# Kernel optimization log

Hardware: AMD Instinct MI355X
Metric: run time of the kernel (lower is better)

Reference implementation:

```python
import jax, jax.numpy as jnp
from jax import lax
import numpy as np

NUM_COEFF = 24      # solver.num_coeff_per_dim (Chebyshev coefficients)
NUM_POINTS = 48     # Chebyshev-Gauss collocation nodes per interval
PICARD_ITERS = 5    # fixed-point iterations of the spectral PAN solve


def _cheb_setup(dtype):
    j = jnp.arange(NUM_POINTS, dtype=dtype)
    n = jnp.arange(NUM_COEFF, dtype=dtype)
    # tau_j = cos(pi*(j+1/2)/P); T[n, j] = T_n(tau_j) = cos(n*arccos(tau_j))
    ang = jnp.pi * (j + 0.5) / NUM_POINTS
    T = jnp.cos(n[:, None] * ang[None, :])                  # [C, P]
    V = (2.0 / NUM_POINTS) * T
    V = V.at[0].mul(0.5)                                    # DCT: a_n = sum_j f(tau_j) V[n, j]
    signs = jnp.cos(n * jnp.pi)                             # T_n(-1) = (-1)^n
    return T, V, signs


def _cheb_antiderivative(a, signs):
    # Chebyshev coeffs of int_{-1}^{tau} f, given coeffs a of f: b_n = (a_{n-1}-a_{n+1})/(2n)
    C = a.shape[-1]
    a_pad = jnp.concatenate([a, jnp.zeros_like(a[..., :2])], axis=-1)
    n = jnp.arange(1, C, dtype=a.dtype)
    b_rest = (a_pad[..., 0:C - 1] - a_pad[..., 2:C + 1]) / (2.0 * n)
    b0 = -jnp.sum(b_rest * signs[1:], axis=-1, keepdims=True)  # enforce value 0 at tau=-1
    return jnp.concatenate([b0, b_rest], axis=-1)


def _vf(y, W1, b1, W2, b2):
    # neural vector field f(t, y): autonomous MLP
    return jnp.tanh(y @ W1 + b1) @ W2 + b2


def _pan_solve(y_init, t_span, W1, b1, W2, b2):
    # Chebyshev-spectral (PAN) ODE solve; returns trajectory at t_span points
    # and the per-interval coefficient tensors B_all [I, batch, dim, C]
    T, V, signs = _cheb_setup(y_init.dtype)

    def solve_interval(y0, ts):
        t0, t1 = ts[0], ts[1]
        scale = (t1 - t0) * 0.5                             # dtau -> dt Jacobian

        def picard(B, _):
            y_nodes = jnp.einsum('bdc,cp->pbd', B, T)       # y at collocation nodes
            fvals = _vf(y_nodes, W1, b1, W2, b2)            # [P, batch, dim]
            a = jnp.einsum('pbd,cp->bdc', fvals, V)         # Chebyshev coeffs of f
            Bn = scale * _cheb_antiderivative(a, signs)
            Bn = Bn.at[..., 0].add(y0)                      # y(tau=-1) = y0
            return Bn, None

        B0 = jnp.zeros((*y0.shape, NUM_COEFF), y0.dtype).at[..., 0].set(y0)
        B, _ = lax.scan(picard, B0, None, length=PICARD_ITERS)
        y1 = jnp.sum(B, axis=-1)                            # T_n(1) = 1
        return y1, (B, y1)

    ts = jnp.stack([t_span[:-1], t_span[1:]], axis=-1)      # [I, 2]
    _, (B_all, y_ends) = lax.scan(solve_interval, y_init, ts)
    traj = jnp.concatenate([y_init[None], y_ends], axis=0)  # [I+1, batch, dim]
    return traj, B_all


def setup_inputs() -> dict:
    key = jax.random.key(0)
    k1, k2, k3 = jax.random.split(key, 3)
    batch, dim, hidden = 256, 512, 512
    s = np.float32(1.0 / np.sqrt(dim))
    return {
        'y_init': jax.random.normal(k1, (batch, dim), jnp.float32),
        't_span': jnp.linspace(0.0, 1.0, 7, dtype=jnp.float32),
        'W1': s * jax.random.normal(k2, (dim, hidden), jnp.float32),
        'b1': jnp.zeros((hidden,), jnp.float32),
        'W2': s * jax.random.normal(k3, (hidden, dim), jnp.float32),
        'b2': jnp.zeros((dim,), jnp.float32),
    }


def reference(y_init, t_span, W1, b1, W2, b2):
    traj, _B_all = _pan_solve(y_init, t_span, W1, b1, W2, b2)
    return (t_span, traj)
```

## Files before the change

kernel.cpp:

```cpp
#include <hip/hip_runtime.h>
#include <hip/hip_bf16.h>
#include <math.h>

#define NC 24
#define NP 48
#define NI 6
#define BATCH 256
#define DIM 512
#define NROW (NP*BATCH)
#define NELEM (BATCH*DIM)

typedef __bf16 bf16x8 __attribute__((ext_vector_type(8)));
typedef float f32x4 __attribute__((ext_vector_type(4)));
using bf16 = __hip_bfloat16;

struct bq8 { __hip_bfloat162 a, b; };

__device__ __forceinline__ void gld_lds16(const void* g, void* l) {
  __builtin_amdgcn_global_load_lds(
      (const __attribute__((address_space(1))) void*)g,
      (__attribute__((address_space(3))) void*)l, 16, 0, 0);
}

__device__ __forceinline__ float fast_tanh(float x) {
  float u = __expf(2.0f * x);
  float r = __builtin_amdgcn_rcpf(u + 1.0f);
  return __builtin_fmaf(-2.0f, r, 1.0f);
}

__global__ void k_setup(const float* __restrict__ t_span, bf16* __restrict__ Mbf,
                        float* __restrict__ wv, float* __restrict__ rs,
                        float* __restrict__ scales, float* __restrict__ zbias,
                        float* __restrict__ out) {
  __shared__ double Tsh[NC][NP];
  __shared__ float Msh[NP][NP];
  __shared__ float wsh[NP];
  int tid = threadIdx.x;
  for (int idx = tid; idx < NC*NP; idx += 64) {
    int c = idx / NP, p = idx % NP;
    Tsh[c][p] = cos((double)c * (M_PI * ((double)p + 0.5) / NP));
  }
  for (int idx = tid; idx < NP*64; idx += 64)
    Mbf[idx] = __float2bfloat16(0.f);
  __syncthreads();
  if (tid < NP) {
    int q = tid;
    double V[NC], K[NC];
    for (int c = 0; c < NC; c++) V[c] = (2.0/NP) * Tsh[c][q];
    V[0] *= 0.5;
    double s = 0.0;
    for (int n = 1; n < NC; n++) {
      double hi = (n+1 < NC) ? V[n+1] : 0.0;
      K[n] = (V[n-1] - hi) / (2.0*n);
      s += (n & 1) ? -K[n] : K[n];
    }
    K[0] = -s;
    double wsum = 0.0;
    for (int c = 0; c < NC; c++) wsum += K[c];
    wv[q] = (float)wsum;
    wsh[q] = (float)wsum;
    for (int p = 0; p < NP; p++) {
      double m = 0.0;
      for (int c = 0; c < NC; c++) m += Tsh[c][p] * K[c];
      Msh[p][q] = (float)m;
      Mbf[p*64 + q] = __float2bfloat16((float)m);
    }
  }
  __syncthreads();
  if (tid < NP) {
    float s = 0.f;
    for (int q = 0; q < NP; q++) s += Msh[tid][q];
    rs[tid] = s;
  }
  if (tid == 0) {
    float s = 0.f;
    for (int q = 0; q < NP; q++) s += wsh[q];
    scales[6] = s;
  }
  for (int idx = tid; idx < DIM; idx += 64) zbias[idx] = 0.f;
  if (tid < NI) scales[tid] = 0.5f*(t_span[tid+1]-t_span[tid]);
  if (tid < NI+1) out[tid] = t_span[tid];
}

__global__ void k_wt(const float* __restrict__ W1, const float* __restrict__ W2,
                     bf16* __restrict__ W1T, bf16* __restrict__ W2T,
                     bf16* __restrict__ W2bf) {
  int idx = blockIdx.x*256 + threadIdx.x;
  int k = idx >> 9, n = idx & 511;
  W1T[n*DIM + k] = __float2bfloat16(W1[idx]);
  W2T[n*DIM + k] = __float2bfloat16(W2[idx]);
  W2bf[idx]      = __float2bfloat16(W2[idx]);
}

__global__ void k_bb(const float* __restrict__ W1, const float* __restrict__ b2,
                     float* __restrict__ bb) {
  int h = blockIdx.x*256 + threadIdx.x;
  float s = 0.f;
  for (int d = 0; d < DIM; d++) s = fmaf(b2[d], W1[d*DIM + h], s);
  bb[h] = s;
}

__global__ void k_init(const float* __restrict__ y_init, float* __restrict__ y0,
                       bf16* __restrict__ y0bf, float* __restrict__ traj0) {
  int i = blockIdx.x*256 + threadIdx.x;
  float v = y_init[i];
  y0[i] = v; traj0[i] = v;
  y0bf[i] = __float2bfloat16(v);
}

template<int EPI>
__global__ __launch_bounds__(256, 3) void k_gemm(const bf16* __restrict__ A,
    const bf16* __restrict__ BT, const float* __restrict__ bias,
    bf16* __restrict__ outb, float* __restrict__ outf) {
  __shared__ bf16 sA[2][128*64];
  __shared__ bf16 sB[2][64*64];
  int tid = threadIdx.x;
  int lane = tid & 63, wid = tid >> 6;
  int q8 = gridDim.x >> 3;
  int tl = (blockIdx.x & 7)*q8 + (blockIdx.x >> 3);
  int bm = tl >> 3, bn = tl & 7;
  int row0 = bm*128, col0 = bn*64;
  int wr = wid >> 1, wc = wid & 1;
  int r16 = lane & 15, g = lane >> 4;

  f32x4 acc[4][2];
  #pragma unroll
  for (int m = 0; m < 4; m++)
    #pragma unroll
    for (int n = 0; n < 2; n++)
      acc[m][n] = {0.f, 0.f, 0.f, 0.f};

  auto stage = [&](int buf, int k0) {
    #pragma unroll
    for (int j = 0; j < 4; j++) {
      int cid = wid*64 + lane + j*256;
      int r = cid >> 3;
      int c = (cid & 7) ^ (r & 7);
      gld_lds16(A + (size_t)(row0 + r)*DIM + k0 + c*8,
                (char*)&sA[buf][0] + wid*1024 + j*4096);
    }
    #pragma unroll
    for (int j = 0; j < 2; j++) {
      int cid = wid*64 + lane + j*256;
      int r = cid >> 3;
      int c = (cid & 7) ^ (r & 7);
      gld_lds16(BT + (size_t)(col0 + r)*DIM + k0 + c*8,
                (char*)&sB[buf][0] + wid*1024 + j*4096);
    }
  };

  stage(0, 0);
  int cur = 0;
  for (int k0 = 0; k0 < DIM; k0 += 64) {
    if (k0 + 64 < DIM) {
      stage(cur ^ 1, k0 + 64);
      asm volatile("s_waitcnt vmcnt(6)" ::: "memory");
    } else {
      asm volatile("s_waitcnt vmcnt(0)" ::: "memory");
    }
    __builtin_amdgcn_s_barrier();
    #pragma unroll
    for (int kk = 0; kk < 2; kk++) {
      bf16x8 af[4], bfr[2];
      #pragma unroll
      for (int m = 0; m < 4; m++) {
        int r = wr*64 + m*16 + r16;
        af[m] = *(const bf16x8*)(&sA[cur][0] + r*64 + (((kk*4+g) ^ (r&7))*8));
      }
      #pragma unroll
      for (int n = 0; n < 2; n++) {
        int r = wc*32 + n*16 + r16;
        bfr[n] = *(const bf16x8*)(&sB[cur][0] + r*64 + (((kk*4+g) ^ (r&7))*8));
      }
      #pragma unroll
      for (int m = 0; m < 4; m++)
        #pragma unroll
        for (int n = 0; n < 2; n++)
          acc[m][n] = __builtin_amdgcn_mfma_f32_16x16x32_bf16(af[m], bfr[n], acc[m][n], 0, 0, 0);
    }
    __builtin_amdgcn_s_barrier();
    cur ^= 1;
  }

  #pragma unroll
  for (int m = 0; m < 4; m++) {
    int rowb = row0 + wr*64 + m*16 + g*4;
    #pragma unroll
    for (int n = 0; n < 2; n++) {
      int col = col0 + wc*32 + n*16 + r16;
      float bv = bias[col];
      #pragma unroll
      for (int r = 0; r < 4; r++) {
        float v = acc[m][n][r] + bv;
        size_t idx = (size_t)(rowb + r)*DIM + col;
        if constexpr (EPI == 1) {
          outb[idx] = __float2bfloat16(v);
        } else {
          outf[idx] = v;
          outb[idx] = __float2bfloat16(fast_tanh(v));
        }
      }
    }
  }
}

template<int FIN>
__global__ __launch_bounds__(256, 2) void k_fused(const bf16* __restrict__ H,
    const bf16* __restrict__ W21T, const float* __restrict__ C,
    const bf16* __restrict__ Mbf, const float* __restrict__ rs,
    const float* __restrict__ bb, const float* __restrict__ wv,
    const float* __restrict__ scales, int t, bf16* __restrict__ outp) {
  __shared__ char smem[57344];
  bf16* sA = (bf16*)smem;
  bf16* sB = (bf16*)(smem + 24576);
  char* sGT = smem;
  int tid = threadIdx.x;
  int lane = tid & 63, wid = tid >> 6;
  int q8 = gridDim.x >> 3;
  int tl = (blockIdx.x & 7)*q8 + (blockIdx.x >> 3);
  int bm = tl >> 2, bn = tl & 3;
  int row0 = bm*96, col0 = bn*128;
  int b_w = wid >> 1;
  int wr0 = b_w*48, wc0 = (wid & 1)*64;
  int r16 = lane & 15, g = lane >> 4;

  bf16x8 af2[3][2];
  #pragma unroll
  for (int pt = 0; pt < 3; pt++)
    #pragma unroll
    for (int kk = 0; kk < 2; kk++)
      af2[pt][kk] = *(const bf16x8*)(Mbf + (pt*16 + r16)*64 + kk*32 + g*8);

  f32x4 acc[3][4];
  #pragma unroll
  for (int m = 0; m < 3; m++)
    #pragma unroll
    for (int n = 0; n < 4; n++)
      acc[m][n] = {0.f, 0.f, 0.f, 0.f};

  auto stage = [&](int buf, int k0) {
    #pragma unroll
    for (int j = 0; j < 3; j++) {
      int cid = j*256 + tid;
      int r = cid >> 3;
      int c = (cid & 7) ^ (r & 7);
      gld_lds16(H + (size_t)(row0 + r)*DIM + k0 + c*8,
                (char*)(sA + buf*6144) + j*4096 + wid*1024);
    }
    #pragma unroll
    for (int j = 0; j < 4; j++) {
      int cid = j*256 + tid;
      int r = cid >> 3;
      int c = (cid & 7) ^ (r & 7);
      gld_lds16(W21T + (size_t)(col0 + r)*DIM + k0 + c*8,
                (char*)(sB + buf*8192) + j*4096 + wid*1024);
    }
  };

  stage(0, 0);
  int cur = 0;
  for (int k0 = 0; k0 < DIM; k0 += 64) {
    if (k0 + 64 < DIM) {
      stage(cur ^ 1, k0 + 64);
      asm volatile("s_waitcnt vmcnt(7)" ::: "memory");
    } else {
      asm volatile("s_waitcnt vmcnt(0)" ::: "memory");
    }
    __builtin_amdgcn_s_barrier();
    #pragma unroll
    for (int kk = 0; kk < 2; kk++) {
      bf16x8 af[3], bfr[4];
      #pragma unroll
      for (int m = 0; m < 3; m++) {
        int r = wr0 + m*16 + r16;
        af[m] = *(const bf16x8*)(sA + cur*6144 + r*64 + (((kk*4+g) ^ (r&7))*8));
      }
      #pragma unroll
      for (int n = 0; n < 4; n++) {
        int r = wc0 + n*16 + r16;
        bfr[n] = *(const bf16x8*)(sB + cur*8192 + r*64 + (((kk*4+g) ^ (r&7))*8));
      }
      #pragma unroll
      for (int m = 0; m < 3; m++)
        #pragma unroll
        for (int n = 0; n < 4; n++)
          acc[m][n] = __builtin_amdgcn_mfma_f32_16x16x32_bf16(af[m], bfr[n], acc[m][n], 0, 0, 0);
    }
    __builtin_amdgcn_s_barrier();
    cur ^= 1;
  }

  __syncthreads();
  #pragma unroll
  for (int m = 0; m < 3; m++) {
    int qb = m*16 + g*4;
    #pragma unroll
    for (int n = 0; n < 4; n++) {
      int h_loc = wc0 + n*16 + r16;
      int ad = (h_loc*256 + b_w*128 + qb*2) ^ ((h_loc&7)<<4);
      bq8 v;
      v.a = __hip_bfloat162{__float2bfloat16(acc[m][n][0]), __float2bfloat16(acc[m][n][1])};
      v.b = __hip_bfloat162{__float2bfloat16(acc[m][n][2]), __float2bfloat16(acc[m][n][3])};
      *(bq8*)(sGT + ad) = v;
    }
  }
  {
    int hz = tid >> 1, bz = tid & 1;
    bq8 z; z.a = __hip_bfloat162{__float2bfloat16(0.f), __float2bfloat16(0.f)}; z.b = z.a;
    #pragma unroll
    for (int j = 0; j < 4; j++) {
      int ad = (hz*256 + bz*128 + 96 + j*8) ^ ((hz&7)<<4);
      *(bq8*)(sGT + ad) = z;
    }
  }
  __syncthreads();

  int hh = wid & 1;
  f32x4 acc2[3][4];
  #pragma unroll
  for (int m = 0; m < 3; m++)
    #pragma unroll
    for (int n = 0; n < 4; n++)
      acc2[m][n] = {0.f, 0.f, 0.f, 0.f};
  #pragma unroll
  for (int kk = 0; kk < 2; kk++) {
    bf16x8 bfr2[4];
    #pragma unroll
    for (int n2 = 0; n2 < 4; n2++) {
      int h_loc = hh*64 + n2*16 + r16;
      int ad = (h_loc*256 + b_w*128 + (kk*32 + g*8)*2) ^ ((h_loc&7)<<4);
      bfr2[n2] = *(const bf16x8*)(sGT + ad);
    }
    #pragma unroll
    for (int pt = 0; pt < 3; pt++)
      #pragma unroll
      for (int n2 = 0; n2 < 4; n2++)
        acc2[pt][n2] = __builtin_amdgcn_mfma_f32_16x16x32_bf16(af2[pt][kk], bfr2[n2], acc2[pt][n2], 0, 0, 0);
  }

  float sc = scales[t];
  int bglob = bm*2 + b_w;
  float rsv[3][4];
  #pragma unroll
  for (int pt = 0; pt < 3; pt++)
    #pragma unroll
    for (int r = 0; r < 4; r++)
      rsv[pt][r] = rs[pt*16 + g*4 + r];

  #pragma unroll
  for (int n2 = 0; n2 < 4; n2++) {
    int h_glob = col0 + hh*64 + n2*16 + r16;
    float cv = C[(size_t)bglob*DIM + h_glob];
    float bbv = bb[h_glob];
    if constexpr (FIN == 0) {
      #pragma unroll
      for (int pt = 0; pt < 3; pt++) {
        #pragma unroll
        for (int r = 0; r < 4; r++) {
          int p = pt*16 + g*4 + r;
          float z = fmaf(sc, fmaf(rsv[pt][r], bbv, acc2[pt][n2][r]), cv);
          outp[((size_t)bglob*NP + p)*DIM + h_glob] = __float2bfloat16(fast_tanh(z));
        }
      }
    } else {
      float hw = 0.f;
      #pragma unroll
      for (int pt = 0; pt < 3; pt++) {
        #pragma unroll
        for (int r = 0; r < 4; r++) {
          int p = pt*16 + g*4 + r;
          float z = fmaf(sc, fmaf(rsv[pt][r], bbv, acc2[pt][n2][r]), cv);
          hw = fmaf(wv[p], fast_tanh(z), hw);
        }
      }
      hw += __shfl_xor(hw, 16);
      hw += __shfl_xor(hw, 32);
      if (g == 0)
        outp[(size_t)bglob*DIM + h_glob] = __float2bfloat16(hw);
    }
  }
}

__global__ __launch_bounds__(256, 3) void k_next(const bf16* __restrict__ A,
    const bf16* __restrict__ W2T, const bf16* __restrict__ W21T,
    const float* __restrict__ b2, const float* __restrict__ bb,
    float* __restrict__ y0, bf16* __restrict__ y0bf, float* __restrict__ C,
    bf16* __restrict__ H1, const float* __restrict__ scales, int t,
    float* __restrict__ traj) {
  __shared__ bf16 sA[2][128*64];
  __shared__ bf16 sB[2][64*64];
  int tid = threadIdx.x;
  int lane = tid & 63, wid = tid >> 6;
  int q8 = gridDim.x >> 3;
  int tl = (blockIdx.x & 7)*q8 + (blockIdx.x >> 3);
  int bm = tl >> 4, bn = tl & 15;
  int half = bn >> 3;
  int row0 = bm*128, col0 = (bn & 7)*64;
  const bf16* BT = half ? W21T : W2T;
  int wr = wid >> 1, wc = wid & 1;
  int r16 = lane & 15, g = lane >> 4;

  f32x4 acc[4][2];
  #pragma unroll
  for (int m = 0; m < 4; m++)
    #pragma unroll
    for (int n = 0; n < 2; n++)
      acc[m][n] = {0.f, 0.f, 0.f, 0.f};

  auto stage = [&](int buf, int k0) {
    #pragma unroll
    for (int j = 0; j < 4; j++) {
      int cid = wid*64 + lane + j*256;
      int r = cid >> 3;
      int c = (cid & 7) ^ (r & 7);
      gld_lds16(A + (size_t)(row0 + r)*DIM + k0 + c*8,
                (char*)&sA[buf][0] + wid*1024 + j*4096);
    }
    #pragma unroll
    for (int j = 0; j < 2; j++) {
      int cid = wid*64 + lane + j*256;
      int r = cid >> 3;
      int c = (cid & 7) ^ (r & 7);
      gld_lds16(BT + (size_t)(col0 + r)*DIM + k0 + c*8,
                (char*)&sB[buf][0] + wid*1024 + j*4096);
    }
  };

  stage(0, 0);
  int cur = 0;
  for (int k0 = 0; k0 < DIM; k0 += 64) {
    if (k0 + 64 < DIM) {
      stage(cur ^ 1, k0 + 64);
      asm volatile("s_waitcnt vmcnt(6)" ::: "memory");
    } else {
      asm volatile("s_waitcnt vmcnt(0)" ::: "memory");
    }
    __builtin_amdgcn_s_barrier();
    #pragma unroll
    for (int kk = 0; kk < 2; kk++) {
      bf16x8 af[4], bfr[2];
      #pragma unroll
      for (int m = 0; m < 4; m++) {
        int r = wr*64 + m*16 + r16;
        af[m] = *(const bf16x8*)(&sA[cur][0] + r*64 + (((kk*4+g) ^ (r&7))*8));
      }
      #pragma unroll
      for (int n = 0; n < 2; n++) {
        int r = wc*32 + n*16 + r16;
        bfr[n] = *(const bf16x8*)(&sB[cur][0] + r*64 + (((kk*4+g) ^ (r&7))*8));
      }
      #pragma unroll
      for (int m = 0; m < 4; m++)
        #pragma unroll
        for (int n = 0; n < 2; n++)
          acc[m][n] = __builtin_amdgcn_mfma_f32_16x16x32_bf16(af[m], bfr[n], acc[m][n], 0, 0, 0);
    }
    __builtin_amdgcn_s_barrier();
    cur ^= 1;
  }

  float sc = scales[t];
  float sumw = scales[6];
  #pragma unroll
  for (int m = 0; m < 4; m++) {
    int rowb = row0 + wr*64 + m*16 + g*4;
    #pragma unroll
    for (int n = 0; n < 2; n++) {
      int col = col0 + wc*32 + n*16 + r16;
      #pragma unroll
      for (int r = 0; r < 4; r++) {
        size_t idx = (size_t)(rowb + r)*DIM + col;
        if (half == 0) {
          float bv = sumw * b2[col];
          float y1 = fmaf(sc, acc[m][n][r] + bv, y0[idx]);
          y0[idx] = y1;
          y0bf[idx] = __float2bfloat16(y1);
          traj[idx] = y1;
        } else {
          float cb = sc * sumw * bb[col];
          float cnew = fmaf(sc, acc[m][n][r], C[idx] + cb);
          C[idx] = cnew;
          H1[idx] = __float2bfloat16(fast_tanh(cnew));
        }
      }
    }
  }
}

__global__ __launch_bounds__(256) void k_combine1(const bf16* __restrict__ G1,
    const float* __restrict__ C, const float* __restrict__ rs,
    const float* __restrict__ bb, const float* __restrict__ scales, int t,
    bf16* __restrict__ outH) {
  int i = (blockIdx.x*256 + threadIdx.x)*2;
  int b = i >> 9, h = i & (DIM-1);
  __hip_bfloat162 gb = *(const __hip_bfloat162*)(G1 + i);
  float2 c = *(const float2*)(C + i);
  float g0 = __bfloat162float(gb.x) + bb[h];
  float g1 = __bfloat162float(gb.y) + bb[h+1];
  float sc = scales[t];
  #pragma unroll
  for (int p = 0; p < NP; p++) {
    float w = sc * rs[p];
    __hip_bfloat162 o;
    o.x = __float2bfloat16(fast_tanh(fmaf(w, g0, c.x)));
    o.y = __float2bfloat16(fast_tanh(fmaf(w, g1, c.y)));
    *(__hip_bfloat162*)(outH + ((size_t)b*NP + p)*DIM + h) = o;
  }
}

extern "C" void kernel_launch(void* const* d_in, const int* in_sizes, int n_in,
                              void* d_out, int out_size, void* d_ws, size_t ws_size,
                              hipStream_t stream) {
  const float* y_init = (const float*)d_in[0];
  const float* t_span = (const float*)d_in[1];
  const float* W1 = (const float*)d_in[2];
  const float* b1 = (const float*)d_in[3];
  const float* W2 = (const float*)d_in[4];
  const float* b2 = (const float*)d_in[5];
  float* out = (float*)d_out;

  char* ws = (char*)d_ws;
  size_t off = 0;
  auto carve = [&](size_t bytes) {
    void* p = ws + off; off += (bytes + 255) & ~(size_t)255; return p;
  };
  bf16*  Mbf    = (bf16*) carve((size_t)NP*64*2);
  float* wv     = (float*)carve(NP*4);
  float* rs     = (float*)carve(NP*4);
  float* bb     = (float*)carve(DIM*4);
  float* scales = (float*)carve(8*4);
  float* zbias  = (float*)carve(DIM*4);
  float* y0     = (float*)carve((size_t)NELEM*4);
  float* C      = (float*)carve((size_t)NELEM*4);
  bf16*  y0bf   = (bf16*) carve((size_t)NELEM*2);
  bf16*  H1     = (bf16*) carve((size_t)NELEM*2);
  bf16*  G1     = (bf16*) carve((size_t)NELEM*2);
  bf16*  Hw     = (bf16*) carve((size_t)NELEM*2);
  bf16*  W1T    = (bf16*) carve((size_t)DIM*DIM*2);
  bf16*  W2T    = (bf16*) carve((size_t)DIM*DIM*2);
  bf16*  W2bf   = (bf16*) carve((size_t)DIM*DIM*2);
  bf16*  W21T   = (bf16*) carve((size_t)DIM*DIM*2);
  bf16*  Ha     = (bf16*) carve((size_t)NROW*DIM*2);
  bf16*  Hb     = (bf16*) carve((size_t)NROW*DIM*2);

  k_setup<<<1, 64, 0, stream>>>(t_span, Mbf, wv, rs, scales, zbias, out);
  k_wt<<<(DIM*DIM)/256, 256, 0, stream>>>(W1, W2, W1T, W2T, W2bf);
  k_bb<<<2, 256, 0, stream>>>(W1, b2, bb);
  k_gemm<1><<<32, 256, 0, stream>>>(W1T, W2bf, zbias, W21T, nullptr);
  k_init<<<NELEM/256, 256, 0, stream>>>(y_init, y0, y0bf, out + 7);
  k_gemm<2><<<16, 256, 0, stream>>>(y0bf, W1T, b1, H1, C);

  const int GRID_FUSED = (NROW/96)*(DIM/128);

  for (int t = 0; t < NI; t++) {
    k_gemm<1><<<16, 256, 0, stream>>>(H1, W21T, zbias, G1, nullptr);
    k_combine1<<<NELEM/512, 256, 0, stream>>>(G1, C, rs, bb, scales, t, Ha);
    k_fused<0><<<GRID_FUSED, 256, 0, stream>>>(Ha, W21T, C, Mbf, rs, bb, wv, scales, t, Hb);
    k_fused<0><<<GRID_FUSED, 256, 0, stream>>>(Hb, W21T, C, Mbf, rs, bb, wv, scales, t, Ha);
    k_fused<1><<<GRID_FUSED, 256, 0, stream>>>(Ha, W21T, C, Mbf, rs, bb, wv, scales, t, Hw);
    k_next<<<32, 256, 0, stream>>>(Hw, W2T, W21T, b2, bb, y0, y0bf, C, H1,
                                   scales, t, out + 7 + (size_t)(t+1)*NELEM);
  }
}
```

Baseline: 469.9 us.

## Fuse per-interval Picard iterations into one per-batch LDS-resident kernel

```diff
diff --git a/kernel.cpp b/kernel.cpp
--- a/kernel.cpp
+++ b/kernel.cpp
@@ -204,25 +204,22 @@
   }
 }
 
-template<int FIN>
-__global__ __launch_bounds__(256, 2) void k_fused(const bf16* __restrict__ H,
-    const bf16* __restrict__ W21T, const float* __restrict__ C,
-    const bf16* __restrict__ Mbf, const float* __restrict__ rs,
-    const float* __restrict__ bb, const float* __restrict__ wv,
-    const float* __restrict__ scales, int t, bf16* __restrict__ outp) {
-  __shared__ char smem[57344];
-  bf16* sA = (bf16*)smem;
-  bf16* sB = (bf16*)(smem + 24576);
-  char* sGT = smem;
+__global__ __launch_bounds__(512, 2) void k_picard(
+    const bf16* __restrict__ H1, const bf16* __restrict__ W21T,
+    const float* __restrict__ C, const bf16* __restrict__ Mbf,
+    const float* __restrict__ rs, const float* __restrict__ bb,
+    const float* __restrict__ wv, const float* __restrict__ scales, int t,
+    bf16* __restrict__ Hw) {
+  extern __shared__ char smem[];
+  char* Hb  = smem;
+  char* sGT = smem + 49152;
+  float* Cb  = (float*)(smem + 114688);
+  float* bbb = (float*)(smem + 116736);
+  int b = blockIdx.x;
   int tid = threadIdx.x;
   int lane = tid & 63, wid = tid >> 6;
-  int q8 = gridDim.x >> 3;
-  int tl = (blockIdx.x & 7)*q8 + (blockIdx.x >> 3);
-  int bm = tl >> 2, bn = tl & 3;
-  int row0 = bm*96, col0 = bn*128;
-  int b_w = wid >> 1;
-  int wr0 = b_w*48, wc0 = (wid & 1)*64;
   int r16 = lane & 15, g = lane >> 4;
+  float sc = scales[t];
 
   bf16x8 af2[3][2];
   #pragma unroll
@@ -230,154 +227,134 @@
     #pragma unroll
     for (int kk = 0; kk < 2; kk++)
       af2[pt][kk] = *(const bf16x8*)(Mbf + (pt*16 + r16)*64 + kk*32 + g*8);
-
-  f32x4 acc[3][4];
-  #pragma unroll
-  for (int m = 0; m < 3; m++)
-    #pragma unroll
-    for (int n = 0; n < 4; n++)
-      acc[m][n] = {0.f, 0.f, 0.f, 0.f};
-
-  auto stage = [&](int buf, int k0) {
-    #pragma unroll
-    for (int j = 0; j < 3; j++) {
-      int cid = j*256 + tid;
-      int r = cid >> 3;
-      int c = (cid & 7) ^ (r & 7);
-      gld_lds16(H + (size_t)(row0 + r)*DIM + k0 + c*8,
-                (char*)(sA + buf*6144) + j*4096 + wid*1024);
-    }
-    #pragma unroll
-    for (int j = 0; j < 4; j++) {
-      int cid = j*256 + tid;
-      int r = cid >> 3;
-      int c = (cid & 7) ^ (r & 7);
-      gld_lds16(W21T + (size_t)(col0 + r)*DIM + k0 + c*8,
-                (char*)(sB + buf*8192) + j*4096 + wid*1024);
-    }
-  };
-
-  stage(0, 0);
-  int cur = 0;
-  for (int k0 = 0; k0 < DIM; k0 += 64) {
-    if (k0 + 64 < DIM) {
-      stage(cur ^ 1, k0 + 64);
-      asm volatile("s_waitcnt vmcnt(7)" ::: "memory");
-    } else {
-      asm volatile("s_waitcnt vmcnt(0)" ::: "memory");
-    }
-    __builtin_amdgcn_s_barrier();
-    #pragma unroll
-    for (int kk = 0; kk < 2; kk++) {
-      bf16x8 af[3], bfr[4];
-      #pragma unroll
-      for (int m = 0; m < 3; m++) {
-        int r = wr0 + m*16 + r16;
-        af[m] = *(const bf16x8*)(sA + cur*6144 + r*64 + (((kk*4+g) ^ (r&7))*8));
-      }
-      #pragma unroll
-      for (int n = 0; n < 4; n++) {
-        int r = wc0 + n*16 + r16;
-        bfr[n] = *(const bf16x8*)(sB + cur*8192 + r*64 + (((kk*4+g) ^ (r&7))*8));
-      }
-      #pragma unroll
-      for (int m = 0; m < 3; m++)
-        #pragma unroll
-        for (int n = 0; n < 4; n++)
-          acc[m][n] = __builtin_amdgcn_mfma_f32_16x16x32_bf16(af[m], bfr[n], acc[m][n], 0, 0, 0);
-    }
-    __builtin_amdgcn_s_barrier();
-    cur ^= 1;
-  }
-
-  __syncthreads();
-  #pragma unroll
-  for (int m = 0; m < 3; m++) {
-    int qb = m*16 + g*4;
-    #pragma unroll
-    for (int n = 0; n < 4; n++) {
-      int h_loc = wc0 + n*16 + r16;
-      int ad = (h_loc*256 + b_w*128 + qb*2) ^ ((h_loc&7)<<4);
-      bq8 v;
-      v.a = __hip_bfloat162{__float2bfloat16(acc[m][n][0]), __float2bfloat16(acc[m][n][1])};
-      v.b = __hip_bfloat162{__float2bfloat16(acc[m][n][2]), __float2bfloat16(acc[m][n][3])};
-      *(bq8*)(sGT + ad) = v;
-    }
-  }
-  {
-    int hz = tid >> 1, bz = tid & 1;
-    bq8 z; z.a = __hip_bfloat162{__float2bfloat16(0.f), __float2bfloat16(0.f)}; z.b = z.a;
-    #pragma unroll
-    for (int j = 0; j < 4; j++) {
-      int ad = (hz*256 + bz*128 + 96 + j*8) ^ ((hz&7)<<4);
-      *(bq8*)(sGT + ad) = z;
-    }
-  }
-  __syncthreads();
-
-  int hh = wid & 1;
-  f32x4 acc2[3][4];
-  #pragma unroll
-  for (int m = 0; m < 3; m++)
-    #pragma unroll
-    for (int n = 0; n < 4; n++)
-      acc2[m][n] = {0.f, 0.f, 0.f, 0.f};
-  #pragma unroll
-  for (int kk = 0; kk < 2; kk++) {
-    bf16x8 bfr2[4];
-    #pragma unroll
-    for (int n2 = 0; n2 < 4; n2++) {
-      int h_loc = hh*64 + n2*16 + r16;
-      int ad = (h_loc*256 + b_w*128 + (kk*32 + g*8)*2) ^ ((h_loc&7)<<4);
-      bfr2[n2] = *(const bf16x8*)(sGT + ad);
-    }
-    #pragma unroll
-    for (int pt = 0; pt < 3; pt++)
-      #pragma unroll
-      for (int n2 = 0; n2 < 4; n2++)
-        acc2[pt][n2] = __builtin_amdgcn_mfma_f32_16x16x32_bf16(af2[pt][kk], bfr2[n2], acc2[pt][n2], 0, 0, 0);
-  }
-
-  float sc = scales[t];
-  int bglob = bm*2 + b_w;
-  float rsv[3][4];
+  float rsv[12], wvv[12];
   #pragma unroll
   for (int pt = 0; pt < 3; pt++)
     #pragma unroll
-    for (int r = 0; r < 4; r++)
-      rsv[pt][r] = rs[pt*16 + g*4 + r];
-
-  #pragma unroll
-  for (int n2 = 0; n2 < 4; n2++) {
-    int h_glob = col0 + hh*64 + n2*16 + r16;
-    float cv = C[(size_t)bglob*DIM + h_glob];
-    float bbv = bb[h_glob];
-    if constexpr (FIN == 0) {
-      #pragma unroll
-      for (int pt = 0; pt < 3; pt++) {
-        #pragma unroll
-        for (int r = 0; r < 4; r++) {
-          int p = pt*16 + g*4 + r;
-          float z = fmaf(sc, fmaf(rsv[pt][r], bbv, acc2[pt][n2][r]), cv);
-          outp[((size_t)bglob*NP + p)*DIM + h_glob] = __float2bfloat16(fast_tanh(z));
+    for (int r = 0; r < 4; r++) {
+      rsv[pt*4+r] = rs[pt*16 + g*4 + r];
+      wvv[pt*4+r] = wv[pt*16 + g*4 + r];
+    }
+
+  Cb[tid] = C[(size_t)b*DIM + tid];
+  bbb[tid] = bb[tid];
+  {
+    bf16 h1 = H1[(size_t)b*DIM + tid];
+    #pragma unroll
+    for (int q = 0; q < NP; q++)
+      *(bf16*)(Hb + q*1024 + ((tid*2) ^ ((q&7)<<4))) = h1;
+  }
+  {
+    int h = tid;
+    bq8 z; z.a = __hip_bfloat162{__float2bfloat16(0.f), __float2bfloat16(0.f)}; z.b = z.a;
+    *(bq8*)(sGT + h*128 + (96  ^ ((h&7)<<4)))     = z;
+    *(bq8*)(sGT + h*128 + (96  ^ ((h&7)<<4)) + 8) = z;
+    *(bq8*)(sGT + h*128 + (112 ^ ((h&7)<<4)))     = z;
+    *(bq8*)(sGT + h*128 + (112 ^ ((h&7)<<4)) + 8) = z;
+  }
+  __syncthreads();
+
+  const bf16* wbase = W21T + (size_t)(wid*16 + r16)*DIM;
+
+  for (int it = 0; it < 4; it++) {
+    f32x4 acc[3][4];
+    #pragma unroll
+    for (int m = 0; m < 3; m++)
+      #pragma unroll
+      for (int hb = 0; hb < 4; hb++)
+        acc[m][hb] = {0.f, 0.f, 0.f, 0.f};
+
+    #pragma unroll
+    for (int ks = 0; ks < 8; ks++) {
+      #pragma unroll
+      for (int kk = 0; kk < 2; kk++) {
+        bf16x8 af[3];
+        #pragma unroll
+        for (int m = 0; m < 3; m++) {
+          int q = m*16 + r16;
+          af[m] = *(const bf16x8*)(Hb + q*1024 +
+                   ((ks*128 + kk*64 + g*16) ^ ((q&7)<<4)));
         }
+        #pragma unroll
+        for (int hb = 0; hb < 4; hb++) {
+          bf16x8 bf = *(const bf16x8*)(wbase + (size_t)hb*128*DIM + ks*64 + kk*32 + g*8);
+          #pragma unroll
+          for (int m = 0; m < 3; m++)
+            acc[m][hb] = __builtin_amdgcn_mfma_f32_16x16x32_bf16(af[m], bf, acc[m][hb], 0, 0, 0);
+        }
+      }
+    }
+    #pragma unroll
+    for (int hb = 0; hb < 4; hb++) {
+      int h = hb*128 + wid*16 + r16;
+      #pragma unroll
+      for (int m = 0; m < 3; m++) {
+        int ad = h*128 + (((m*32 + g*8)) ^ ((h&7)<<4));
+        bq8 v;
+        v.a = __hip_bfloat162{__float2bfloat16(acc[m][hb][0]), __float2bfloat16(acc[m][hb][1])};
+        v.b = __hip_bfloat162{__float2bfloat16(acc[m][hb][2]), __float2bfloat16(acc[m][hb][3])};
+        *(bq8*)(sGT + ad) = v;
+      }
+    }
+    __syncthreads();
+
+    f32x4 acc2[3][4];
+    #pragma unroll
+    for (int pt = 0; pt < 3; pt++)
+      #pragma unroll
+      for (int n2 = 0; n2 < 4; n2++)
+        acc2[pt][n2] = {0.f, 0.f, 0.f, 0.f};
+    #pragma unroll
+    for (int kk = 0; kk < 2; kk++) {
+      bf16x8 bfr2[4];
+      #pragma unroll
+      for (int n2 = 0; n2 < 4; n2++) {
+        int h = wid*64 + n2*16 + r16;
+        bfr2[n2] = *(const bf16x8*)(sGT + h*128 + ((kk*64 + g*16) ^ ((h&7)<<4)));
+      }
+      #pragma unroll
+      for (int pt = 0; pt < 3; pt++)
+        #pragma unroll
+        for (int n2 = 0; n2 < 4; n2++)
+          acc2[pt][n2] = __builtin_amdgcn_mfma_f32_16x16x32_bf16(af2[pt][kk], bfr2[n2], acc2[pt][n2], 0, 0, 0);
+    }
+
+    if (it < 3) {
+      #pragma unroll
+      for (int n2 = 0; n2 < 4; n2++) {
+        int h = wid*64 + n2*16 + r16;
+        float cv = Cb[h], bbv = bbb[h];
+        #pragma unroll
+        for (int pt = 0; pt < 3; pt++) {
+          #pragma unroll
+          for (int r = 0; r < 4; r++) {
+            int p = pt*16 + g*4 + r;
+            float z = fmaf(sc, fmaf(rsv[pt*4+r], bbv, acc2[pt][n2][r]), cv);
+            *(bf16*)(Hb + p*1024 + ((h*2) ^ ((p&7)<<4))) = __float2bfloat16(fast_tanh(z));
+          }
+        }
       }
     } else {
-      float hw = 0.f;
-      #pragma unroll
-      for (int pt = 0; pt < 3; pt++) {
-        #pragma unroll
-        for (int r = 0; r < 4; r++) {
-          int p = pt*16 + g*4 + r;
-          float z = fmaf(sc, fmaf(rsv[pt][r], bbv, acc2[pt][n2][r]), cv);
-          hw = fmaf(wv[p], fast_tanh(z), hw);
+      #pragma unroll
+      for (int n2 = 0; n2 < 4; n2++) {
+        int h = wid*64 + n2*16 + r16;
+        float cv = Cb[h], bbv = bbb[h];
+        float hw = 0.f;
+        #pragma unroll
+        for (int pt = 0; pt < 3; pt++) {
+          #pragma unroll
+          for (int r = 0; r < 4; r++) {
+            float z = fmaf(sc, fmaf(rsv[pt*4+r], bbv, acc2[pt][n2][r]), cv);
+            hw = fmaf(wvv[pt*4+r], fast_tanh(z), hw);
+          }
         }
-      }
-      hw += __shfl_xor(hw, 16);
-      hw += __shfl_xor(hw, 32);
-      if (g == 0)
-        outp[(size_t)bglob*DIM + h_glob] = __float2bfloat16(hw);
-    }
+        hw += __shfl_xor(hw, 16);
+        hw += __shfl_xor(hw, 32);
+        if (g == 0)
+          Hw[(size_t)b*DIM + h] = __float2bfloat16(hw);
+      }
+    }
+    __syncthreads();
   }
 }
 
@@ -487,27 +464,6 @@
   }
 }
 
-__global__ __launch_bounds__(256) void k_combine1(const bf16* __restrict__ G1,
-    const float* __restrict__ C, const float* __restrict__ rs,
-    const float* __restrict__ bb, const float* __restrict__ scales, int t,
-    bf16* __restrict__ outH) {
-  int i = (blockIdx.x*256 + threadIdx.x)*2;
-  int b = i >> 9, h = i & (DIM-1);
-  __hip_bfloat162 gb = *(const __hip_bfloat162*)(G1 + i);
-  float2 c = *(const float2*)(C + i);
-  float g0 = __bfloat162float(gb.x) + bb[h];
-  float g1 = __bfloat162float(gb.y) + bb[h+1];
-  float sc = scales[t];
-  #pragma unroll
-  for (int p = 0; p < NP; p++) {
-    float w = sc * rs[p];
-    __hip_bfloat162 o;
-    o.x = __float2bfloat16(fast_tanh(fmaf(w, g0, c.x)));
-    o.y = __float2bfloat16(fast_tanh(fmaf(w, g1, c.y)));
-    *(__hip_bfloat162*)(outH + ((size_t)b*NP + p)*DIM + h) = o;
-  }
-}
-
 extern "C" void kernel_launch(void* const* d_in, const int* in_sizes, int n_in,
                               void* d_out, int out_size, void* d_ws, size_t ws_size,
                               hipStream_t stream) {
@@ -534,14 +490,15 @@
   float* C      = (float*)carve((size_t)NELEM*4);
   bf16*  y0bf   = (bf16*) carve((size_t)NELEM*2);
   bf16*  H1     = (bf16*) carve((size_t)NELEM*2);
-  bf16*  G1     = (bf16*) carve((size_t)NELEM*2);
   bf16*  Hw     = (bf16*) carve((size_t)NELEM*2);
   bf16*  W1T    = (bf16*) carve((size_t)DIM*DIM*2);
   bf16*  W2T    = (bf16*) carve((size_t)DIM*DIM*2);
   bf16*  W2bf   = (bf16*) carve((size_t)DIM*DIM*2);
   bf16*  W21T   = (bf16*) carve((size_t)DIM*DIM*2);
-  bf16*  Ha     = (bf16*) carve((size_t)NROW*DIM*2);
-  bf16*  Hb     = (bf16*) carve((size_t)NROW*DIM*2);
+
+  const int MEGA_LDS = 118784;
+  hipFuncSetAttribute(reinterpret_cast<const void*>(&k_picard),
+                      hipFuncAttributeMaxDynamicSharedMemorySize, MEGA_LDS);
 
   k_setup<<<1, 64, 0, stream>>>(t_span, Mbf, wv, rs, scales, zbias, out);
   k_wt<<<(DIM*DIM)/256, 256, 0, stream>>>(W1, W2, W1T, W2T, W2bf);
@@ -550,14 +507,9 @@
   k_init<<<NELEM/256, 256, 0, stream>>>(y_init, y0, y0bf, out + 7);
   k_gemm<2><<<16, 256, 0, stream>>>(y0bf, W1T, b1, H1, C);
 
-  const int GRID_FUSED = (NROW/96)*(DIM/128);
-
   for (int t = 0; t < NI; t++) {
-    k_gemm<1><<<16, 256, 0, stream>>>(H1, W21T, zbias, G1, nullptr);
-    k_combine1<<<NELEM/512, 256, 0, stream>>>(G1, C, rs, bb, scales, t, Ha);
-    k_fused<0><<<GRID_FUSED, 256, 0, stream>>>(Ha, W21T, C, Mbf, rs, bb, wv, scales, t, Hb);
-    k_fused<0><<<GRID_FUSED, 256, 0, stream>>>(Hb, W21T, C, Mbf, rs, bb, wv, scales, t, Ha);
-    k_fused<1><<<GRID_FUSED, 256, 0, stream>>>(Ha, W21T, C, Mbf, rs, bb, wv, scales, t, Hw);
+    k_picard<<<BATCH, 512, MEGA_LDS, stream>>>(H1, W21T, C, Mbf, rs, bb, wv,
+                                               scales, t, Hw);
     k_next<<<32, 256, 0, stream>>>(Hw, W2T, W21T, b2, bb, y0, y0bf, C, H1,
                                    scales, t, out + 7 + (size_t)(t+1)*NELEM);
   }
```

Measured after the change: 790.4 us. 68.2% more time.
